# Optimization experiments

Hardware: AMD Instinct MI355X
Metric: run time of the kernel (lower is better)

## Reference

```python
import jax, jax.numpy as jnp
import numpy as np
import itertools
from jax import lax

B, F, T = 4096, 10, 480
NW, W = 24, 20          # 24 windows of width 20 (index_list = [0,20,...,480])
HID = 64                 # GRU hidden size
NLAYERS = 2
PAIRS = np.array(list(itertools.combinations(range(F), 2)))  # [45,2]
P = PAIRS.shape[0]
D_IN = 2 * P + 12 * F    # GRU input size = 210
BN_EPS = 1e-5


def setup_inputs() -> dict:
    key = jax.random.key(0)
    ks = jax.random.split(key, 16)
    s = 0.1
    g = 1.0 / np.sqrt(HID)
    inp = {
        "data": jax.random.normal(ks[0], (B, 1, F, T), jnp.float32),
        "conv_w": 1.0 + s * jax.random.normal(ks[1], (), jnp.float32),
        "conv_b": s * jax.random.normal(ks[2], (), jnp.float32),
        "bn_gamma": 1.0 + s * jax.random.normal(ks[3], (14,), jnp.float32),
        "bn_beta": s * jax.random.normal(ks[4], (14,), jnp.float32),
        "gru_Wih0": g * jax.random.normal(ks[5], (3 * HID, D_IN), jnp.float32),
        "gru_Whh0": g * jax.random.normal(ks[6], (3 * HID, HID), jnp.float32),
        "gru_bih0": g * jax.random.normal(ks[7], (3 * HID,), jnp.float32),
        "gru_bhh0": g * jax.random.normal(ks[8], (3 * HID,), jnp.float32),
        "gru_Wih1": g * jax.random.normal(ks[9], (3 * HID, HID), jnp.float32),
        "gru_Whh1": g * jax.random.normal(ks[10], (3 * HID, HID), jnp.float32),
        "gru_bih1": g * jax.random.normal(ks[11], (3 * HID,), jnp.float32),
        "gru_bhh1": g * jax.random.normal(ks[12], (3 * HID,), jnp.float32),
        "comb_a": jnp.asarray(PAIRS[:, 0], jnp.int32),
        "comb_b": jnp.asarray(PAIRS[:, 1], jnp.int32),
    }
    return inp


def _gru_layer(x_seq, Wih, Whh, bih, bhh):
    # x_seq: [B, S, D]
    b = x_seq.shape[0]
    h0 = jnp.zeros((b, HID), x_seq.dtype)

    def step(h, xt):
        gi = xt @ Wih.T + bih           # [B, 3H]
        gh = h @ Whh.T + bhh
        i_r, i_z, i_n = jnp.split(gi, 3, axis=-1)
        h_r, h_z, h_n = jnp.split(gh, 3, axis=-1)
        r = jax.nn.sigmoid(i_r + h_r)
        z = jax.nn.sigmoid(i_z + h_z)
        n = jnp.tanh(i_n + r * h_n)
        h_new = (1.0 - z) * n + z * h
        return h_new, h_new

    hT, ys = lax.scan(step, h0, jnp.swapaxes(x_seq, 0, 1))
    return jnp.swapaxes(ys, 0, 1), hT


def reference(data, conv_w, conv_b, bn_gamma, bn_beta,
              gru_Wih0, gru_Whh0, gru_bih0, gru_bhh0,
              gru_Wih1, gru_Whh1, gru_bih1, gru_bhh1,
              comb_a, comb_b):
    b = data.shape[0]
    # uniform index_list -> reshape time into [NW, W] windows
    x = data[:, 0].reshape(b, F, NW, W)            # [B, F, NW, W]
    mean = x.mean(-1)                              # [B, F, NW]
    cen = x - mean[..., None]
    var = (cen * cen).mean(-1)                     # population var (np.std default)
    std = jnp.sqrt(var)
    m3 = (cen ** 3).mean(-1)
    m4 = (cen ** 4).mean(-1)

    # pairwise cov / corr over feature combinations
    xa = x[:, comb_a]                              # [B, P, NW, W]
    xb = x[:, comb_b]
    ca = xa - mean[:, comb_a][..., None]
    cb = xb - mean[:, comb_b][..., None]
    cov = (ca * cb).sum(-1) / (W - 1)              # [B, P, NW]
    corr = cov / (std[:, comb_a] * std[:, comb_b] + 0.01)

    dec_w = (jnp.arange(1, W + 1, dtype=x.dtype) / (W * (W + 1) / 2.0))
    stats = [
        corr,                                      # 1 ts_corr
        cov,                                       # 2 ts_cov
        std,                                       # 3 ts_stddev
        mean / (std + 0.01),                       # 4 ts_zscore
        x[..., -1] / (x[..., 0] + 0.01) - 1.0,     # 5 ts_return
        (x * dec_w).sum(-1),                       # 6 ts_decaylinear
        mean,                                      # 7 ts_mean
        x.min(-1),                                 # 8 ts_min
        var,                                       # 9 ts_var
        x.sum(-1),                                 # 10 ts_sum
        jnp.median(x, axis=-1),                    # 11 ts_median
        m3 / (std ** 3 + 0.01),                    # 12 ts_skew
        m4 / (std ** 4 + 0.01) - 3.0,              # 13 ts_kurtosis
        x.sum(-1),                                 # 14 ts_sum (again)
    ]

    # 1x1 conv (scalar affine, shared) + per-stat BatchNorm2d(1) in training mode
    outs = []
    for i, s_ in enumerate(stats):
        y = conv_w * s_ + conv_b
        m = y.mean()
        v = y.var()
        outs.append(bn_gamma[i] * (y - m) * lax.rsqrt(v + BN_EPS) + bn_beta[i])
    feat = jnp.concatenate(outs, axis=1)           # [B, D_IN, NW]
    seq = jnp.swapaxes(feat, 1, 2)                 # [B, NW, D_IN]

    ys0, _ = _gru_layer(seq, gru_Wih0, gru_Whh0, gru_bih0, gru_bhh0)
    _, h1 = _gru_layer(ys0, gru_Wih1, gru_Whh1, gru_bih1, gru_bhh1)
    return h1                                      # [B, HID]
```

## Files before the change

### kernel.cpp

```cpp
#include <hip/hip_runtime.h>
#include <math.h>

#define NF 10
#define TLEN 480
#define NWIN 24
#define WLEN 20
#define HID 64
#define NPAIR 45
#define DIN 210
#define NG 14
#define GATES 192
#define NGRP 256
#define FROW 212
#define XROW 484
#define NB 4096
#define NW2 16384

typedef __attribute__((ext_vector_type(8))) short bf16x8;
typedef __attribute__((ext_vector_type(4))) float f32x4;

#define MFMA(a,b,c) __builtin_amdgcn_mfma_f32_16x16x32_bf16((a),(b),(c),0,0,0)

__device__ __forceinline__ int grp_of(int k){ return (k < 90) ? (k / 45) : 2 + (k - 90) / 10; }

__device__ __forceinline__ void split2(float x, short& hi, short& lo){
    unsigned u = __float_as_uint(x);
    hi = (short)(u >> 16);
    float hf = __uint_as_float(u & 0xffff0000u);
    lo = (short)(__float_as_uint(x - hf) >> 16);
}
__device__ __forceinline__ short bf16rne(float x){
    unsigned u = __float_as_uint(x);
    u += 0x7fffu + ((u >> 16) & 1u);
    return (short)(u >> 16);
}
__device__ __forceinline__ float sigm(float x){
    return __builtin_amdgcn_rcpf(1.f + __builtin_amdgcn_exp2f(x * -1.4426950408889634f));
}
__device__ __forceinline__ float tanhfast(float x){
    return 1.f - 2.f * __builtin_amdgcn_rcpf(1.f + __builtin_amdgcn_exp2f(x * 2.8853900817779268f));
}

__global__ __launch_bounds__(256)
void stats_kernel(const float* __restrict__ data, float* __restrict__ feat32,
                  float* __restrict__ part1, float* __restrict__ part2)
{
    __shared__ __align__(16) float xs[NF * XROW];
    __shared__ float ts[NWIN][121];
    __shared__ float sgs[NG], sgq[NG];
    int b = blockIdx.x, tid = threadIdx.x;
    const float* src = data + (size_t)b * (NF * TLEN);

    for (int q = tid; q < 1200; q += 256){
        int f = q / 120, r = q % 120;
        *(float4*)&xs[f * XROW + r * 4] = *(const float4*)&src[q * 4];
    }
    if (tid < NG){ sgs[tid] = 0.f; sgq[tid] = 0.f; }
    __syncthreads();

    if (tid < 240){
        int f = tid / NWIN, t = tid % NWIN;
        const float* p = &xs[f * XROW + t * WLEN];
        float v[WLEN];
        {
            float4 a0 = *(const float4*)(p + 0);
            float4 a1 = *(const float4*)(p + 4);
            float4 a2 = *(const float4*)(p + 8);
            float4 a3 = *(const float4*)(p + 12);
            float4 a4 = *(const float4*)(p + 16);
            v[0]=a0.x; v[1]=a0.y; v[2]=a0.z; v[3]=a0.w;
            v[4]=a1.x; v[5]=a1.y; v[6]=a1.z; v[7]=a1.w;
            v[8]=a2.x; v[9]=a2.y; v[10]=a2.z; v[11]=a2.w;
            v[12]=a3.x; v[13]=a3.y; v[14]=a3.z; v[15]=a3.w;
            v[16]=a4.x; v[17]=a4.y; v[18]=a4.z; v[19]=a4.w;
        }
        float sum = 0.f, wsum = 0.f;
        #pragma unroll
        for (int i = 0; i < WLEN; ++i){
            sum += v[i];
            wsum += v[i] * ((float)(i + 1) * (1.0f / 210.0f));
        }
        float mean = sum * (1.0f / WLEN);
        float var = 0.f, m3 = 0.f, m4 = 0.f;
        #pragma unroll
        for (int i = 0; i < WLEN; ++i){
            float c = v[i] - mean, c2 = c * c;
            var += c2; m3 += c2 * c; m4 += c2 * c2;
        }
        var *= 0.05f; m3 *= 0.05f; m4 *= 0.05f;
        float sd = sqrtf(var);
        float ratio = v[WLEN - 1] / (v[0] + 0.01f) - 1.0f;

        #pragma unroll
        for (int rr = 0; rr < 10; ++rr){
            #pragma unroll
            for (int i = (rr & 1); i + 1 < 10; i += 2){
                float lo0 = fminf(v[i], v[i + 1]);
                float hi0 = fmaxf(v[i], v[i + 1]);
                v[i] = lo0; v[i + 1] = hi0;
                float lo1 = fminf(v[10 + i], v[10 + i + 1]);
                float hi1 = fmaxf(v[10 + i], v[10 + i + 1]);
                v[10 + i] = lo1; v[10 + i + 1] = hi1;
            }
        }
        float Lmax = fminf(v[0], v[19]);
        float Hmin = fmaxf(v[0], v[19]);
        #pragma unroll
        for (int i = 1; i < 10; ++i){
            float li = fminf(v[i], v[19 - i]);
            float hi2 = fmaxf(v[i], v[19 - i]);
            Lmax = fmaxf(Lmax, li);
            Hmin = fminf(Hmin, hi2);
        }
        float median = 0.5f * (Lmax + Hmin);
        float minv = fminf(v[0], v[10]);
        float s3 = sd * sd * sd;
        float mos = mean / (sd + 0.01f);
        float skew = m3 / (s3 + 0.01f);
        float kurt = m4 / (s3 * sd + 0.01f) - 3.0f;

        ts[t][  0 + f] = sd;
        ts[t][ 10 + f] = mos;
        ts[t][ 20 + f] = ratio;
        ts[t][ 30 + f] = wsum;
        ts[t][ 40 + f] = mean;
        ts[t][ 50 + f] = minv;
        ts[t][ 60 + f] = var;
        ts[t][ 70 + f] = sum;
        ts[t][ 80 + f] = median;
        ts[t][ 90 + f] = skew;
        ts[t][100 + f] = kurt;
        ts[t][110 + f] = sum;
    }
    __syncthreads();

    size_t grp = b >> 4, e = b & 15;

    {
        int w = tid >> 6, l = tid & 63;
        int f = l & 15, kb = l >> 4;
        float cs = 0.f, cq = 0.f, vs2 = 0.f, vq = 0.f;
        #pragma unroll 1
        for (int s = 0; s < 6; ++s){
            int nw = w * 6 + s;
            float vv[8];
            #pragma unroll
            for (int j = 0; j < 8; ++j) vv[j] = 0.f;
            if (f < NF && kb < 3){
                const float* p = &xs[f * XROW + nw * WLEN + kb * 8];
                float4 u0 = *(const float4*)p;
                vv[0] = u0.x; vv[1] = u0.y; vv[2] = u0.z; vv[3] = u0.w;
                if (kb < 2){
                    float4 u1 = *(const float4*)(p + 4);
                    vv[4] = u1.x; vv[5] = u1.y; vv[6] = u1.z; vv[7] = u1.w;
                }
            }
            bf16x8 Fh, Fl;
            #pragma unroll
            for (int j = 0; j < 8; ++j){ short hi, lo; split2(vv[j], hi, lo); Fh[j] = hi; Fl[j] = lo; }
            f32x4 g = {0.f, 0.f, 0.f, 0.f};
            g = MFMA(Fh, Fh, g);
            g = MFMA(Fh, Fl, g);
            g = MFMA(Fl, Fh, g);
            size_t base = ((grp * NWIN + nw) * 16 + e) * FROW;
            #pragma unroll
            for (int i = 0; i < 4; ++i){
                int fa = kb * 4 + i, fb = f;
                if (fa < fb && fb < NF){
                    float ma = ts[nw][40 + fa], mb = ts[nw][40 + fb];
                    float sa = ts[nw][0 + fa],  sb = ts[nw][0 + fb];
                    float cov = (g[i] - (float)WLEN * ma * mb) * (1.0f / (WLEN - 1));
                    float corr = cov / (sa * sb + 0.01f);
                    int pi = (((19 - fa) * fa) >> 1) + fb - fa - 1;
                    feat32[base + pi] = corr;
                    feat32[base + NPAIR + pi] = cov;
                    cs += corr; cq += corr * corr;
                    vs2 += cov; vq += cov * cov;
                }
            }
        }
        float acc[4] = {cs, cq, vs2, vq};
        int wid = b * 4 + w;
        #pragma unroll
        for (int j = 0; j < 4; ++j){
            float a = acc[j];
            #pragma unroll
            for (int m = 1; m < 64; m <<= 1) a += __shfl_xor(a, m);
            if (l == 0) part2[(size_t)j * NW2 + wid] = a;
        }
    }

    if (tid < 120){
        int g = 2 + tid / 10;
        float s = 0.f, q = 0.f;
        #pragma unroll
        for (int t = 0; t < NWIN; ++t){
            float v = ts[t][tid];
            s += v; q += v * v;
        }
        atomicAdd(&sgs[g], s);
        atomicAdd(&sgq[g], q);
    }
    __syncthreads();

    if (tid < 24){
        int j = tid >> 1, wh = tid & 1;
        part1[(size_t)tid * NB + b] = wh ? sgq[2 + j] : sgs[2 + j];
    }
    for (int q = tid; q < NWIN * 120; q += 256){
        int t = q / 120, c = q % 120;
        size_t base = ((grp * NWIN + t) * 16 + e) * FROW;
        feat32[base + 90 + c] = ts[t][c];
    }
    if (tid < 48){
        int t = tid >> 1;
        size_t base = ((grp * NWIN + t) * 16 + e) * FROW;
        feat32[base + 210 + (tid & 1)] = 0.f;
    }
}

__global__ __launch_bounds__(256)
void reduce_kernel(const float* __restrict__ part1, const float* __restrict__ part2,
                   float* __restrict__ accum)
{
    __shared__ float red[256];
    int j = blockIdx.x;
    int g = j % NG, which = j / NG;
    const float* base; int n;
    if (g < 2){ base = part2 + (size_t)(g * 2 + which) * NW2; n = NW2; }
    else      { base = part1 + (size_t)((g - 2) * 2 + which) * NB; n = NB; }
    int tid = threadIdx.x;
    float s = 0.f;
    for (int i = tid; i < n; i += 256) s += base[i];
    red[tid] = s; __syncthreads();
    for (int step = 128; step > 0; step >>= 1){
        if (tid < step) red[tid] += red[tid + step];
        __syncthreads();
    }
    if (tid == 0) accum[which * NG + g] = red[0];
}

__global__ __launch_bounds__(256)
void prep_kernel(const float* __restrict__ Wih0, const float* __restrict__ Whh0,
                 const float* __restrict__ Wih1, const float* __restrict__ Whh1,
                 const float* __restrict__ bih0, const float* __restrict__ accum,
                 const float* __restrict__ conv_w, const float* __restrict__ bn_gamma,
                 const float* __restrict__ bn_beta,
                 short* __restrict__ WHh, short* __restrict__ W0h, float* __restrict__ bf0)
{
    __shared__ float scs[NG], shs[NG];
    int tid = threadIdx.x;
    if (tid < NG){
        float N = (tid < 2) ? 4096.f * NPAIR * NWIN : 4096.f * NF * NWIN;
        float m = accum[tid] / N;
        float v = accum[NG + tid] / N - m * m;
        float cw = conv_w[0];
        float A = bn_gamma[tid] * rsqrtf(cw * cw * v + 1e-5f);
        scs[tid] = A * cw;
        shs[tid] = bn_beta[tid] - A * cw * m;
    }
    __syncthreads();
    const int NH = 3 * 2 * 12 * 64 * 8;
    const int N0 = 7 * 12 * 64 * 8;
    for (int i = blockIdx.x * 256 + tid; i < NH + N0; i += gridDim.x * 256){
        if (i < NH){
            int j = i & 7, lane = (i >> 3) & 63, rest = i >> 9;
            int ct = rest % 12; rest /= 12;
            int ks = rest & 1, m = rest >> 1;
            int gg = ct * 16 + (lane & 15);
            int k = ks * 32 + ((lane >> 4) << 3) + j;
            const float* Wm = (m == 0) ? Whh0 : (m == 1) ? Wih1 : Whh1;
            WHh[i] = bf16rne(Wm[gg * HID + k]);
        } else {
            int e2 = i - NH;
            int j = e2 & 7, lane = (e2 >> 3) & 63, rest = e2 >> 9;
            int ct = rest % 12, ks = rest / 12;
            int gg = ct * 16 + (lane & 15);
            int k = ks * 32 + ((lane >> 4) << 3) + j;
            float v = (k < DIN) ? Wih0[gg * DIN + k] * scs[grp_of(k)] : 0.f;
            W0h[e2] = bf16rne(v);
        }
    }
    if (blockIdx.x == 0 && tid < GATES){
        float s = bih0[tid];
        for (int k = 0; k < DIN; ++k) s += Wih0[tid * DIN + k] * shs[grp_of(k)];
        bf0[tid] = s;
    }
}

__device__ __forceinline__ void stage_fa(short (*fab)[64][8], int tix,
                                         const float* __restrict__ feat32, int ht)
{
    for (int q = ht; q < 448; q += 256){
        int c = q >> 4, e = q & 15;
        float vv[8];
        const float* src = &feat32[((size_t)tix * 16 + e) * FROW + c * 8];
        if (c < 26){
            float4 u0 = *(const float4*)src, u1 = *(const float4*)(src + 4);
            vv[0]=u0.x; vv[1]=u0.y; vv[2]=u0.z; vv[3]=u0.w;
            vv[4]=u1.x; vv[5]=u1.y; vv[6]=u1.z; vv[7]=u1.w;
        } else if (c == 26){
            float4 u0 = *(const float4*)src;
            vv[0]=u0.x; vv[1]=u0.y; vv[2]=u0.z; vv[3]=u0.w;
            vv[4]=0.f; vv[5]=0.f; vv[6]=0.f; vv[7]=0.f;
        } else {
            #pragma unroll
            for (int j = 0; j < 8; ++j) vv[j] = 0.f;
        }
        bf16x8 h8, l8;
        #pragma unroll
        for (int j = 0; j < 8; ++j){ short hi, lo; split2(vv[j], hi, lo); h8[j] = hi; l8[j] = lo; }
        *(bf16x8*)&fab[(c >> 2) * 2 + 0][e + 16 * (c & 3)][0] = h8;
        *(bf16x8*)&fab[(c >> 2) * 2 + 1][e + 16 * (c & 3)][0] = l8;
    }
}

__global__ __launch_bounds__(512, 1)
void rec_kernel(const float* __restrict__ feat32,
                const short* __restrict__ WHh, const short* __restrict__ W0h,
                const float* __restrict__ bf0, const float* __restrict__ bhh0,
                const float* __restrict__ bih1, const float* __restrict__ bhh1,
                float* __restrict__ out)
{
    __shared__ __align__(16) short fa[2][14][64][8];
    __shared__ __align__(16) short hp0[2][2][16][72];
    __shared__ __align__(16) short hp1[2][2][16][72];
    int tid = threadIdx.x;
    int w = tid >> 6, l = tid & 63;
    int lm = l & 15, kb = l >> 4;
    int blk = blockIdx.x;

    for (int i = tid; i < 2 * 2 * 16 * 72; i += 512){
        ((short*)hp0)[i] = 0;
        ((short*)hp1)[i] = 0;
    }
    for (int q = tid; q < 448; q += 512){
        int c = q >> 4, e = q & 15;
        float vv[8];
        const float* src = &feat32[((size_t)(blk * NWIN) * 16 + e) * FROW + c * 8];
        if (c < 26){
            float4 u0 = *(const float4*)src, u1 = *(const float4*)(src + 4);
            vv[0]=u0.x; vv[1]=u0.y; vv[2]=u0.z; vv[3]=u0.w;
            vv[4]=u1.x; vv[5]=u1.y; vv[6]=u1.z; vv[7]=u1.w;
        } else if (c == 26){
            float4 u0 = *(const float4*)src;
            vv[0]=u0.x; vv[1]=u0.y; vv[2]=u0.z; vv[3]=u0.w;
            vv[4]=0.f; vv[5]=0.f; vv[6]=0.f; vv[7]=0.f;
        } else {
            #pragma unroll
            for (int j = 0; j < 8; ++j) vv[j] = 0.f;
        }
        bf16x8 h8, l8;
        #pragma unroll
        for (int j = 0; j < 8; ++j){ short hi, lo; split2(vv[j], hi, lo); h8[j] = hi; l8[j] = lo; }
        *(bf16x8*)&fa[0][(c >> 2) * 2 + 0][e + 16 * (c & 3)][0] = h8;
        *(bf16x8*)&fa[0][(c >> 2) * 2 + 1][e + 16 * (c & 3)][0] = l8;
    }

    if (w < 4){
        int jc = w * 16 + lm;
        bf16x8 WH0_[2][3];
        #pragma unroll
        for (int ks = 0; ks < 2; ++ks)
            #pragma unroll
            for (int ro = 0; ro < 3; ++ro)
                WH0_[ks][ro] = *(const bf16x8*)&WHh[((((0 * 2 + ks) * 12) + (ro * 4 + w)) * 64 + l) * 8];
        bf16x8 W0_[7][3];
        #pragma unroll
        for (int ks = 0; ks < 7; ++ks)
            #pragma unroll
            for (int ro = 0; ro < 3; ++ro)
                W0_[ks][ro] = *(const bf16x8*)&W0h[(((ks * 12) + (ro * 4 + w)) * 64 + l) * 8];

        float cr0 = bf0[jc]       + bhh0[jc];
        float cz0 = bf0[jc + 64]  + bhh0[jc + 64];
        float cin0 = bf0[jc + 128];
        float chn0 = bhh0[jc + 128];
        float h0p[4] = {0.f, 0.f, 0.f, 0.f};

        __syncthreads();
        #pragma unroll 1
        for (int k = 0; k < 25; ++k){
            if (k < 24){
                int rb = (k & 1) ^ 1, wb = k & 1;
                bf16x8 h0h[2], h0l[2];
                #pragma unroll
                for (int ks = 0; ks < 2; ++ks){
                    int off = ks * 32 + kb * 8;
                    h0h[ks] = *(const bf16x8*)&hp0[rb][0][lm][off];
                    h0l[ks] = *(const bf16x8*)&hp0[rb][1][lm][off];
                }
                f32x4 ar0 = {cr0, cr0, cr0, cr0};
                f32x4 az0 = {cz0, cz0, cz0, cz0};
                f32x4 ain0 = {cin0, cin0, cin0, cin0};
                f32x4 ahn0 = {chn0, chn0, chn0, chn0};
                #pragma unroll
                for (int ks = 0; ks < 2; ++ks){
                    ar0 = MFMA(h0h[ks], WH0_[ks][0], ar0);  ar0 = MFMA(h0l[ks], WH0_[ks][0], ar0);
                    az0 = MFMA(h0h[ks], WH0_[ks][1], az0);  az0 = MFMA(h0l[ks], WH0_[ks][1], az0);
                    ahn0 = MFMA(h0h[ks], WH0_[ks][2], ahn0); ahn0 = MFMA(h0l[ks], WH0_[ks][2], ahn0);
                }
                #pragma unroll
                for (int ks = 0; ks < 7; ++ks){
                    bf16x8 Fh = *(const bf16x8*)&fa[k & 1][ks * 2 + 0][l][0];
                    bf16x8 Fl = *(const bf16x8*)&fa[k & 1][ks * 2 + 1][l][0];
                    ar0 = MFMA(Fh, W0_[ks][0], ar0);  ar0 = MFMA(Fl, W0_[ks][0], ar0);
                    az0 = MFMA(Fh, W0_[ks][1], az0);  az0 = MFMA(Fl, W0_[ks][1], az0);
                    ain0 = MFMA(Fh, W0_[ks][2], ain0); ain0 = MFMA(Fl, W0_[ks][2], ain0);
                }
                #pragma unroll
                for (int i = 0; i < 4; ++i){
                    int row = kb * 4 + i;
                    float rg = sigm(ar0[i]);
                    float zg = sigm(az0[i]);
                    float nn = tanhfast(ain0[i] + rg * ahn0[i]);
                    float h = (1.f - zg) * nn + zg * h0p[i];
                    h0p[i] = h;
                    short hi, lo; split2(h, hi, lo);
                    hp0[wb][0][row][jc] = hi;
                    hp0[wb][1][row][jc] = lo;
                }
            }
            __syncthreads();
        }
    } else {
        int w2 = w - 4;
        int jc = w2 * 16 + lm;
        int ht = tid - 256;
        bf16x8 WH1_[2][3], WH2_[2][3];
        #pragma unroll
        for (int ks = 0; ks < 2; ++ks)
            #pragma unroll
            for (int ro = 0; ro < 3; ++ro){
                WH1_[ks][ro] = *(const bf16x8*)&WHh[((((1 * 2 + ks) * 12) + (ro * 4 + w2)) * 64 + l) * 8];
                WH2_[ks][ro] = *(const bf16x8*)&WHh[((((2 * 2 + ks) * 12) + (ro * 4 + w2)) * 64 + l) * 8];
            }
        float cr1 = bih1[jc]      + bhh1[jc];
        float cz1 = bih1[jc + 64] + bhh1[jc + 64];
        float cin1 = bih1[jc + 128];
        float chn1 = bhh1[jc + 128];
        float h1p[4] = {0.f, 0.f, 0.f, 0.f};

        __syncthreads();
        #pragma unroll 1
        for (int k = 0; k < 25; ++k){
            if (k < 23) stage_fa(fa[(k + 1) & 1], blk * NWIN + k + 1, feat32, ht);
            if (k >= 1){
                int t = k - 1;
                int rb0 = t & 1;
                int rh = (k & 1) ^ 1, wh = k & 1;
                bf16x8 n0h[2], n0l[2], h1h[2], h1l[2];
                #pragma unroll
                for (int ks = 0; ks < 2; ++ks){
                    int off = ks * 32 + kb * 8;
                    n0h[ks] = *(const bf16x8*)&hp0[rb0][0][lm][off];
                    n0l[ks] = *(const bf16x8*)&hp0[rb0][1][lm][off];
                    h1h[ks] = *(const bf16x8*)&hp1[rh][0][lm][off];
                    h1l[ks] = *(const bf16x8*)&hp1[rh][1][lm][off];
                }
                f32x4 ar1 = {cr1, cr1, cr1, cr1};
                f32x4 az1 = {cz1, cz1, cz1, cz1};
                f32x4 ain1 = {cin1, cin1, cin1, cin1};
                f32x4 ahn1 = {chn1, chn1, chn1, chn1};
                #pragma unroll
                for (int ks = 0; ks < 2; ++ks){
                    ar1 = MFMA(n0h[ks], WH1_[ks][0], ar1);  ar1 = MFMA(n0l[ks], WH1_[ks][0], ar1);
                    az1 = MFMA(n0h[ks], WH1_[ks][1], az1);  az1 = MFMA(n0l[ks], WH1_[ks][1], az1);
                    ain1 = MFMA(n0h[ks], WH1_[ks][2], ain1); ain1 = MFMA(n0l[ks], WH1_[ks][2], ain1);
                    ar1 = MFMA(h1h[ks], WH2_[ks][0], ar1);  ar1 = MFMA(h1l[ks], WH2_[ks][0], ar1);
                    az1 = MFMA(h1h[ks], WH2_[ks][1], az1);  az1 = MFMA(h1l[ks], WH2_[ks][1], az1);
                    ahn1 = MFMA(h1h[ks], WH2_[ks][2], ahn1); ahn1 = MFMA(h1l[ks], WH2_[ks][2], ahn1);
                }
                #pragma unroll
                for (int i = 0; i < 4; ++i){
                    int row = kb * 4 + i;
                    float rg = sigm(ar1[i]);
                    float zg = sigm(az1[i]);
                    float nn = tanhfast(ain1[i] + rg * ahn1[i]);
                    float h = (1.f - zg) * nn + zg * h1p[i];
                    h1p[i] = h;
                    short hi, lo; split2(h, hi, lo);
                    hp1[wh][0][row][jc] = hi;
                    hp1[wh][1][row][jc] = lo;
                }
            }
            __syncthreads();
        }
        #pragma unroll
        for (int i = 0; i < 4; ++i)
            out[((size_t)(blk * 16) + kb * 4 + i) * HID + jc] = h1p[i];
    }
}

extern "C" void kernel_launch(void* const* d_in, const int* in_sizes, int n_in,
                              void* d_out, int out_size, void* d_ws, size_t ws_size,
                              hipStream_t stream) {
    const float* data     = (const float*)d_in[0];
    const float* conv_w   = (const float*)d_in[1];
    const float* bn_gamma = (const float*)d_in[3];
    const float* bn_beta  = (const float*)d_in[4];
    const float* Wih0     = (const float*)d_in[5];
    const float* Whh0     = (const float*)d_in[6];
    const float* bih0     = (const float*)d_in[7];
    const float* bhh0     = (const float*)d_in[8];
    const float* Wih1     = (const float*)d_in[9];
    const float* Whh1     = (const float*)d_in[10];
    const float* bih1     = (const float*)d_in[11];
    const float* bhh1     = (const float*)d_in[12];
    float* out = (float*)d_out;

    char* ws = (char*)d_ws;
    const size_t feat32_bytes = (size_t)NGRP * NWIN * 16 * FROW * 4;
    const size_t WH_BYTES = 3 * 2 * 12 * 64 * 8 * 2;
    const size_t W0_BYTES = 7 * 12 * 64 * 8 * 2;
    const size_t P1_BYTES = (size_t)24 * NB * 4;

    float* feat32 = (float*)ws;
    short* WHh  = (short*)(ws + feat32_bytes);
    short* W0h  = (short*)(ws + feat32_bytes + WH_BYTES);
    float* bf0  = (float*)(ws + feat32_bytes + WH_BYTES + W0_BYTES);
    float* accum = (float*)(ws + feat32_bytes + WH_BYTES + W0_BYTES + 1024);
    float* part1 = (float*)(ws + feat32_bytes + WH_BYTES + W0_BYTES + 2048);
    float* part2 = (float*)(ws + feat32_bytes + WH_BYTES + W0_BYTES + 2048 + P1_BYTES);

    stats_kernel<<<NB, 256, 0, stream>>>(data, feat32, part1, part2);
    reduce_kernel<<<28, 256, 0, stream>>>(part1, part2, accum);
    prep_kernel<<<64, 256, 0, stream>>>(Wih0, Whh0, Wih1, Whh1, bih0, accum,
                                        conv_w, bn_gamma, bn_beta, WHh, W0h, bf0);
    rec_kernel<<<NGRP, 512, 0, stream>>>(feat32, WHh, W0h, bf0,
                                         bhh0, bih1, bhh1, out);
}
```

Before: 137.3 us.

## Split recurrence blocks to 8 batch rows and prefetch next window into registers

The GRU recurrence kernel now launches twice as many blocks, each handling 8 real batch rows padded to the 16-row MFMA tile, so all CUs get work instead of only 256 blocks. The feature staging loads for window k+2 are issued one iteration early into registers and converted to split-bf16 in LDS on the next step, hiding global latency behind the MFMA work. The cost is that half of every MFMA tile does wasted work on zero rows. Launch bounds are raised to allow more resident blocks per CU, which may limit registers.

```diff
diff --git a/kernel.cpp b/kernel.cpp
--- a/kernel.cpp
+++ b/kernel.cpp
@@ -10,11 +10,11 @@
 #define DIN 210
 #define NG 14
 #define GATES 192
-#define NGRP 256
 #define FROW 212
 #define XROW 484
 #define NB 4096
 #define NW2 16384
+#define RBLK 512
 
 typedef __attribute__((ext_vector_type(8))) short bf16x8;
 typedef __attribute__((ext_vector_type(4))) float f32x4;
@@ -288,34 +288,7 @@
     }
 }
 
-__device__ __forceinline__ void stage_fa(short (*fab)[64][8], int tix,
-                                         const float* __restrict__ feat32, int ht)
-{
-    for (int q = ht; q < 448; q += 256){
-        int c = q >> 4, e = q & 15;
-        float vv[8];
-        const float* src = &feat32[((size_t)tix * 16 + e) * FROW + c * 8];
-        if (c < 26){
-            float4 u0 = *(const float4*)src, u1 = *(const float4*)(src + 4);
-            vv[0]=u0.x; vv[1]=u0.y; vv[2]=u0.z; vv[3]=u0.w;
-            vv[4]=u1.x; vv[5]=u1.y; vv[6]=u1.z; vv[7]=u1.w;
-        } else if (c == 26){
-            float4 u0 = *(const float4*)src;
-            vv[0]=u0.x; vv[1]=u0.y; vv[2]=u0.z; vv[3]=u0.w;
-            vv[4]=0.f; vv[5]=0.f; vv[6]=0.f; vv[7]=0.f;
-        } else {
-            #pragma unroll
-            for (int j = 0; j < 8; ++j) vv[j] = 0.f;
-        }
-        bf16x8 h8, l8;
-        #pragma unroll
-        for (int j = 0; j < 8; ++j){ short hi, lo; split2(vv[j], hi, lo); h8[j] = hi; l8[j] = lo; }
-        *(bf16x8*)&fab[(c >> 2) * 2 + 0][e + 16 * (c & 3)][0] = h8;
-        *(bf16x8*)&fab[(c >> 2) * 2 + 1][e + 16 * (c & 3)][0] = l8;
-    }
-}
-
-__global__ __launch_bounds__(512, 1)
+__global__ __launch_bounds__(512, 4)
 void rec_kernel(const float* __restrict__ feat32,
                 const short* __restrict__ WHh, const short* __restrict__ W0h,
                 const float* __restrict__ bf0, const float* __restrict__ bhh0,
@@ -329,32 +302,34 @@
     int w = tid >> 6, l = tid & 63;
     int lm = l & 15, kb = l >> 4;
     int blk = blockIdx.x;
+    size_t grp = blk >> 1;
+    int ebase = (blk & 1) * 8;
 
     for (int i = tid; i < 2 * 2 * 16 * 72; i += 512){
         ((short*)hp0)[i] = 0;
         ((short*)hp1)[i] = 0;
     }
-    for (int q = tid; q < 448; q += 512){
-        int c = q >> 4, e = q & 15;
+    for (int i = tid; i < 2 * 14 * 64 * 8; i += 512) ((short*)fa)[i] = 0;
+    __syncthreads();
+
+    if (tid < 216){
+        int e8 = tid / 27, c = tid % 27;
+        const float* srcp = &feat32[((grp * NWIN + 0) * 16 + ebase + e8) * FROW + c * 8];
         float vv[8];
-        const float* src = &feat32[((size_t)(blk * NWIN) * 16 + e) * FROW + c * 8];
         if (c < 26){
-            float4 u0 = *(const float4*)src, u1 = *(const float4*)(src + 4);
+            float4 u0 = *(const float4*)srcp, u1 = *(const float4*)(srcp + 4);
             vv[0]=u0.x; vv[1]=u0.y; vv[2]=u0.z; vv[3]=u0.w;
             vv[4]=u1.x; vv[5]=u1.y; vv[6]=u1.z; vv[7]=u1.w;
-        } else if (c == 26){
-            float4 u0 = *(const float4*)src;
+        } else {
+            float4 u0 = *(const float4*)srcp;
             vv[0]=u0.x; vv[1]=u0.y; vv[2]=u0.z; vv[3]=u0.w;
             vv[4]=0.f; vv[5]=0.f; vv[6]=0.f; vv[7]=0.f;
-        } else {
-            #pragma unroll
-            for (int j = 0; j < 8; ++j) vv[j] = 0.f;
         }
         bf16x8 h8, l8;
         #pragma unroll
         for (int j = 0; j < 8; ++j){ short hi, lo; split2(vv[j], hi, lo); h8[j] = hi; l8[j] = lo; }
-        *(bf16x8*)&fa[0][(c >> 2) * 2 + 0][e + 16 * (c & 3)][0] = h8;
-        *(bf16x8*)&fa[0][(c >> 2) * 2 + 1][e + 16 * (c & 3)][0] = l8;
+        *(bf16x8*)&fa[0][(c >> 2) * 2 + 0][e8 + 16 * (c & 3)][0] = h8;
+        *(bf16x8*)&fa[0][(c >> 2) * 2 + 1][e8 + 16 * (c & 3)][0] = l8;
     }
 
     if (w < 4){
@@ -441,10 +416,33 @@
         float chn1 = bhh1[jc + 128];
         float h1p[4] = {0.f, 0.f, 0.f, 0.f};
 
+        int se8 = ht / 27, sc = ht % 27;
+        bool stg = (ht < 216);
+        float4 pr0 = make_float4(0.f,0.f,0.f,0.f), pr1 = make_float4(0.f,0.f,0.f,0.f);
+        if (stg){
+            const float* srcp = &feat32[((grp * NWIN + 1) * 16 + ebase + se8) * FROW + sc * 8];
+            if (sc < 26){ pr0 = *(const float4*)srcp; pr1 = *(const float4*)(srcp + 4); }
+            else        { pr0 = *(const float4*)srcp; }
+        }
         __syncthreads();
+
         #pragma unroll 1
         for (int k = 0; k < 25; ++k){
-            if (k < 23) stage_fa(fa[(k + 1) & 1], blk * NWIN + k + 1, feat32, ht);
+            if (k <= 22 && stg){
+                short (*fab)[64][8] = fa[(k + 1) & 1];
+                float vv[8] = {pr0.x, pr0.y, pr0.z, pr0.w, pr1.x, pr1.y, pr1.z, pr1.w};
+                bf16x8 h8, l8;
+                #pragma unroll
+                for (int j = 0; j < 8; ++j){ short hi, lo; split2(vv[j], hi, lo); h8[j] = hi; l8[j] = lo; }
+                *(bf16x8*)&fab[(sc >> 2) * 2 + 0][se8 + 16 * (sc & 3)][0] = h8;
+                *(bf16x8*)&fab[(sc >> 2) * 2 + 1][se8 + 16 * (sc & 3)][0] = l8;
+            }
+            if (k <= 21 && stg){
+                const float* srcp = &feat32[((grp * NWIN + k + 2) * 16 + ebase + se8) * FROW + sc * 8];
+                pr1 = make_float4(0.f,0.f,0.f,0.f);
+                if (sc < 26){ pr0 = *(const float4*)srcp; pr1 = *(const float4*)(srcp + 4); }
+                else        { pr0 = *(const float4*)srcp; }
+            }
             if (k >= 1){
                 int t = k - 1;
                 int rb0 = t & 1;
@@ -486,9 +484,11 @@
             }
             __syncthreads();
         }
-        #pragma unroll
-        for (int i = 0; i < 4; ++i)
-            out[((size_t)(blk * 16) + kb * 4 + i) * HID + jc] = h1p[i];
+        if (kb < 2){
+            #pragma unroll
+            for (int i = 0; i < 4; ++i)
+                out[((size_t)(blk * 8) + kb * 4 + i) * HID + jc] = h1p[i];
+        }
     }
 }
 
@@ -510,7 +510,7 @@
     float* out = (float*)d_out;
 
     char* ws = (char*)d_ws;
-    const size_t feat32_bytes = (size_t)NGRP * NWIN * 16 * FROW * 4;
+    const size_t feat32_bytes = (size_t)256 * NWIN * 16 * FROW * 4;
     const size_t WH_BYTES = 3 * 2 * 12 * 64 * 8 * 2;
     const size_t W0_BYTES = 7 * 12 * 64 * 8 * 2;
     const size_t P1_BYTES = (size_t)24 * NB * 4;
@@ -527,6 +527,6 @@
     reduce_kernel<<<28, 256, 0, stream>>>(part1, part2, accum);
     prep_kernel<<<64, 256, 0, stream>>>(Wih0, Whh0, Wih1, Whh1, bih0, accum,
                                         conv_w, bn_gamma, bn_beta, WHh, W0h, bf0);
-    rec_kernel<<<NGRP, 512, 0, stream>>>(feat32, WHh, W0h, bf0,
+    rec_kernel<<<RBLK, 512, 0, stream>>>(feat32, WHh, W0h, bf0,
                                          bhh0, bih1, bhh1, out);
 }
```

Result: slower. 176.0 us (+28.2%).
